# Kernel tuning notes

Measured on AMD Instinct MI355X. Metric: run time of the kernel, lower is better.

The kernel has to match this reference:

```python
import jax, jax.numpy as jnp
import numpy as np

Q_DIM = 9   # state(7) + action(2)
KV_DIM = 5  # fixed by get_input_tensors: 4 relative features + r_trans
H = 3
D = KV_DIM * H  # 15


def setup_inputs() -> dict:
    key = jax.random.key(0)
    ks = jax.random.split(key, 16)
    b, t = 32, 256

    def u(k, shape, fan_in):
        lim = (1.0 / fan_in) ** 0.5
        return jax.random.uniform(k, shape, jnp.float32, -lim, lim)

    return {
        "state": jax.random.normal(ks[0], (b, t, 7), jnp.float32),
        "action": jax.random.normal(ks[1], (b, t, 2), jnp.float32),
        "Wk": u(ks[2], (D, KV_DIM), KV_DIM),
        "Wq": u(ks[3], (D, Q_DIM), Q_DIM),
        "Wv": u(ks[4], (D, KV_DIM), KV_DIM),
        "att_bias": jax.random.uniform(ks[5], (KV_DIM,), jnp.float32, -0.1, 0.1),
        "Wscore": u(ks[6], (1, KV_DIM), KV_DIM),
        "bscore": u(ks[7], (1,), KV_DIM),
        "g1": jnp.ones((D,), jnp.float32),
        "beta1": jnp.zeros((D,), jnp.float32),
        "W1": u(ks[8], (5 * D, D), D),
        "bff1": u(ks[9], (5 * D,), D),
        "W2": u(ks[10], (D, 5 * D), 5 * D),
        "bff2": u(ks[11], (D,), 5 * D),
        "g2": jnp.ones((D,), jnp.float32),
        "beta2": jnp.zeros((D,), jnp.float32),
    }


def _layernorm(x, g, b, eps=1e-5):
    m = jnp.mean(x, axis=-1, keepdims=True)
    v = jnp.var(x, axis=-1, keepdims=True)
    return (x - m) * jax.lax.rsqrt(v + eps) * g + b


def _get_input_tensors(state):
    b, t, _ = state.shape
    init = state[..., :4]                                  # (b,t,4)
    rel = init[:, None, :, :] - init[:, :, None, :]        # (b,t,t,4): row i, col j -> s_j - s_i
    xy = rel.reshape(b, t, t, 2, 2).transpose(0, 1, 2, 4, 3)  # [...,0,:]=(x,vx), [...,1,:]=(y,vy)
    ang = -state[..., -1] + 0.5 * jnp.pi                   # (b,t)
    c = jnp.cos(ang)[:, None, :, None]                     # broadcast over row dim -> angle of col j
    s = jnp.sin(ang)[:, None, :, None]
    xr = xy[..., 0, :] * c - xy[..., 1, :] * s             # (b,t,t,2)
    yr = xy[..., 0, :] * s + xy[..., 1, :] * c
    rel = jnp.concatenate([xr, yr], axis=3)                # [xn,vxn,yn,vyn]
    rel = rel.reshape(b, t, t, 2, 2).transpose(0, 1, 2, 4, 3).reshape(b, t, t, 4)  # [xn,yn,vxn,vyn]
    # drop diagonal (j != i) via precomputed off-diagonal column indices
    rows = jnp.arange(t)[:, None]
    j = jnp.arange(t - 1)[None, :]
    cols = j + (j >= rows)                                 # (t,t-1)
    rel = rel[:, rows, cols, :]                            # (b,t,t-1,4)
    r = jnp.sqrt(rel[..., 0] ** 2 + rel[..., 1] ** 2)[..., None]  # (b,t,t-1,1)
    r_trans = 1.0 / (1.0 + jnp.exp(-1.0 + 5.0 * (r - 0.2)))
    kv_x = jnp.concatenate([rel[..., :2] / r, rel[..., 2:], r_trans], axis=-1)  # (b,t,t-1,5)
    return state, kv_x


def reference(state, action, Wk, Wq, Wv, att_bias, Wscore, bscore,
              g1, beta1, W1, bff1, W2, bff2, g2, beta2):
    q_x, kv_x = _get_input_tensors(state)
    q_x = jnp.concatenate([q_x, action], axis=-1)          # (b,t,Q_DIM)
    b, t, tm1, _ = kv_x.shape

    keys = (kv_x @ Wk.T).reshape(b, t, tm1, H, KV_DIM)     # (b,t,t-1,h,k)
    queries = (q_x @ Wq.T).reshape(b, t, 1, H, KV_DIM)
    e = jnp.tanh(keys + queries + att_bias)
    score = (e @ Wscore.T + bscore)[..., 0]                # (b,t,t-1,h)
    values = (kv_x @ Wv.T).reshape(b, t, tm1, H, KV_DIM)
    w = jax.nn.softmax(score, axis=2)                      # softmax over the t-1 neighbours
    x = jnp.einsum('btjh,btjhk->bthk', w, values).reshape(b, t, H * KV_DIM)

    x = _layernorm(x, g1, beta1)
    y = jax.nn.relu(x @ W1.T + bff1) @ W2.T + bff2
    x = x + y
    return _layernorm(x, g2, beta2)
```

## Files before the change

kernel.cpp:

```cpp
#include <hip/hip_runtime.h>
#include <math.h>

#define TT   256
#define TM1  255
#define QD   9
#define KD   5
#define NH   3
#define DD   15
#define HID  75
#define NR   18

__device__ __forceinline__ float fast_rcp(float x) {
    return __builtin_amdgcn_rcpf(x);
}

template<int CTRL>
__device__ __forceinline__ float dpp_add(float x) {
    int y = __builtin_amdgcn_update_dpp(0, __float_as_int(x), CTRL, 0xf, 0xf, true);
    return x + __int_as_float(y);
}

__device__ __forceinline__ float wave_sum63(float x) {
    x = dpp_add<0x111>(x);
    x = dpp_add<0x112>(x);
    x = dpp_add<0x114>(x);
    x = dpp_add<0x118>(x);
    x = dpp_add<0x142>(x);
    x = dpp_add<0x143>(x);
    return x;
}

__device__ __forceinline__ float bcast(float x, int l) {
    return __int_as_float(__builtin_amdgcn_readlane(__float_as_int(x), l));
}

__global__ __launch_bounds__(256)
void fused_block_kernel(const float* __restrict__ state,
                        const float* __restrict__ action,
                        const float* __restrict__ Wk,
                        const float* __restrict__ Wq,
                        const float* __restrict__ Wv,
                        const float* __restrict__ att_bias,
                        const float* __restrict__ Wscore,
                        const float* __restrict__ bscore,
                        const float* __restrict__ g1,
                        const float* __restrict__ beta1,
                        const float* __restrict__ W1,
                        const float* __restrict__ bff1,
                        const float* __restrict__ W2,
                        const float* __restrict__ bff2,
                        const float* __restrict__ g2,
                        const float* __restrict__ beta2,
                        float* __restrict__ out)
{
    const int tid  = threadIdx.x;
    const int lane = tid & 63;
    const int wv   = __builtin_amdgcn_readfirstlane(tid >> 6);
    const int qgrp = blockIdx.x * 4 + wv;
    const int b    = qgrp >> 8;
    const int qi   = qgrp & 255;

    __shared__ float s_h[4][76];

    const float* __restrict__ sb  = state + (size_t)b*TT*7;
    const float* __restrict__ sti = sb + qi*7;
    const float si0 = sti[0], si1 = sti[1], si2 = sti[2], si3 = sti[3];

    float qv = 0.0f;
    if (lane < DD) {
        float acc = att_bias[lane % KD];
        #pragma unroll
        for (int k = 0; k < 7; k++) acc = fmaf(Wq[lane*QD+k], sti[k], acc);
        acc = fmaf(Wq[lane*QD+7], action[((size_t)b*TT+qi)*2 + 0], acc);
        acc = fmaf(Wq[lane*QD+8], action[((size_t)b*TT+qi)*2 + 1], acc);
        qv = acc;
    }
    float qb2[DD];
    #pragma unroll
    for (int d = 0; d < DD; d++) qb2[d] = bcast(qv + qv, d);

    float wsc2[KD];
    float C = bscore[0];
    #pragma unroll
    for (int kk = 0; kk < KD; kk++) { float w = Wscore[kk]; wsc2[kk] = -2.0f*w; C += w; }

    float red[NR];
    #pragma unroll
    for (int n = 0; n < NR; n++) red[n] = 0.0f;

    #pragma unroll
    for (int pp = 0; pp < 4; pp++) {
        const int mm = lane + pp*64;
        if (mm < TM1) {
            const int jj = mm + (mm >= qi ? 1 : 0);
            const float* stj = sb + jj*7;
            const float d0 = stj[0]-si0, d1 = stj[1]-si1;
            const float d2 = stj[2]-si2, d3 = stj[3]-si3;
            const float th = stj[6];
            const float cs = __sinf(th);
            const float sn = __cosf(th);
            const float xr0 = d0*cs - d1*sn, yr0 = d0*sn + d1*cs;
            const float xr1 = d2*cs - d3*sn, yr1 = d2*sn + d3*cs;
            const float s2   = fmaxf(fmaf(xr0, xr0, yr0*yr0), 1e-12f);
            const float rinv = __builtin_amdgcn_rsqf(s2);
            const float r    = s2 * rinv;
            const float rt   = fast_rcp(1.0f + __expf(fmaf(5.0f, r, -2.0f)));
            const float kv0 = xr0*rinv, kv1 = yr0*rinv;
            const float f0 = kv0+kv0, f1 = kv1+kv1, f2 = xr1+xr1,
                        f3 = yr1+yr1, f4 = rt+rt;

            #pragma unroll
            for (int h = 0; h < NH; h++) {
                float sc = C;
                #pragma unroll
                for (int kk = 0; kk < KD; kk++) {
                    const int d = h*KD + kk;
                    float a = qb2[d];
                    a = fmaf(Wk[d*KD+0], f0, a);
                    a = fmaf(Wk[d*KD+1], f1, a);
                    a = fmaf(Wk[d*KD+2], f2, a);
                    a = fmaf(Wk[d*KD+3], f3, a);
                    a = fmaf(Wk[d*KD+4], f4, a);
                    sc = fmaf(wsc2[kk], fast_rcp(__expf(a) + 1.0f), sc);
                }
                const float p = __expf(sc);
                red[h] += p;
                red[NH+h*KD+0] = fmaf(p, kv0, red[NH+h*KD+0]);
                red[NH+h*KD+1] = fmaf(p, kv1, red[NH+h*KD+1]);
                red[NH+h*KD+2] = fmaf(p, xr1, red[NH+h*KD+2]);
                red[NH+h*KD+3] = fmaf(p, yr1, red[NH+h*KD+3]);
                red[NH+h*KD+4] = fmaf(p, rt , red[NH+h*KD+4]);
            }
        }
    }

    #pragma unroll
    for (int n = 0; n < NR; n++) red[n] = wave_sum63(red[n]);
    float fin[NR];
    #pragma unroll
    for (int n = 0; n < NR; n++) fin[n] = bcast(red[n], 63);

    float xm = 0.0f;
    if (lane < DD) {
        const int h = lane / KD;
        float acc = 0.0f;
        #pragma unroll
        for (int c = 0; c < KD; c++) acc = fmaf(Wv[lane*KD+c], fin[NH+h*KD+c], acc);
        xm = acc * fast_rcp(fin[h]);
    }

    float s1 = xm, sq = xm*xm;
    #pragma unroll
    for (int off = 8; off >= 1; off >>= 1) {
        s1 += __shfl_xor(s1, off, 16);
        sq += __shfl_xor(sq, off, 16);
    }
    const float mu1   = s1 * (1.0f/DD);
    const float rstd1 = rsqrtf(sq * (1.0f/DD) - mu1*mu1 + 1e-5f);
    float xln = 0.0f;
    if (lane < DD) xln = (xm - mu1) * rstd1 * g1[lane] + beta1[lane];

    float xs[DD];
    #pragma unroll
    for (int d = 0; d < DD; d++) xs[d] = bcast(xln, d);

    {
        float h0 = bff1[lane];
        #pragma unroll
        for (int k = 0; k < DD; k++) h0 = fmaf(W1[lane*DD+k], xs[k], h0);
        s_h[wv][lane] = fmaxf(h0, 0.0f);
        if (lane < HID-64) {
            float h1 = bff1[lane+64];
            #pragma unroll
            for (int k = 0; k < DD; k++) h1 = fmaf(W1[(lane+64)*DD+k], xs[k], h1);
            s_h[wv][lane+64] = fmaxf(h1, 0.0f);
        }
    }

    const int c2  = lane >> 4;
    const int d2c = lane & 15;
    const int cc  = (c2 < 3) ? c2 : 2;
    const int dc  = (d2c < DD) ? d2c : 0;
    float acc2 = 0.0f;
    #pragma unroll
    for (int k = 0; k < 25; k++)
        acc2 = fmaf(W2[dc*HID + cc*25 + k], s_h[wv][cc*25 + k], acc2);
    acc2 = (c2 < 3) ? acc2 : 0.0f;
    acc2 += __shfl_xor(acc2, 16);
    acc2 += __shfl_xor(acc2, 32);

    float x2 = 0.0f;
    if (lane < DD) x2 = xln + bff2[lane] + acc2;
    float t1 = x2, t2 = x2*x2;
    #pragma unroll
    for (int off = 8; off >= 1; off >>= 1) {
        t1 += __shfl_xor(t1, off, 16);
        t2 += __shfl_xor(t2, off, 16);
    }
    const float mu2   = t1 * (1.0f/DD);
    const float rstd2 = rsqrtf(t2 * (1.0f/DD) - mu2*mu2 + 1e-5f);
    if (lane < DD)
        out[(size_t)qgrp*DD + lane] = (x2 - mu2) * rstd2 * g2[lane] + beta2[lane];
}

extern "C" void kernel_launch(void* const* d_in, const int* in_sizes, int n_in,
                              void* d_out, int out_size, void* d_ws, size_t ws_size,
                              hipStream_t stream) {
    const float* state    = (const float*)d_in[0];
    const float* action   = (const float*)d_in[1];
    const float* Wk       = (const float*)d_in[2];
    const float* Wq       = (const float*)d_in[3];
    const float* Wv       = (const float*)d_in[4];
    const float* att_bias = (const float*)d_in[5];
    const float* Wscore   = (const float*)d_in[6];
    const float* bscore   = (const float*)d_in[7];
    const float* g1       = (const float*)d_in[8];
    const float* beta1    = (const float*)d_in[9];
    const float* W1       = (const float*)d_in[10];
    const float* bff1     = (const float*)d_in[11];
    const float* W2       = (const float*)d_in[12];
    const float* bff2     = (const float*)d_in[13];
    const float* g2       = (const float*)d_in[14];
    const float* beta2    = (const float*)d_in[15];
    float* out = (float*)d_out;

    dim3 grid(32 * 256 / 4);
    dim3 block(256);
    fused_block_kernel<<<grid, block, 0, stream>>>(
        state, action, Wk, Wq, Wv, att_bias, Wscore, bscore,
        g1, beta1, W1, bff1, W2, bff2, g2, beta2, out);
}
```

Before: 27.84 us.

## Fold exp scaling constants into features and hoist neighbor loads out of loop

Pre-scales queries, key features and score weights by 2*log2(e) so every exp becomes a raw v_exp_f32 (exp2) with no per-call multiply. Undoes the scale in the final value normalization. All neighbor state rows are loaded up front and features computed before the main loop. The masked tail lanes now use a large negative score constant instead of a branch. This trims VALU work per element and lets global loads overlap, at the cost of more live registers and a softmax tail contribution of exp2(-100) instead of exactly zero.

```diff
diff --git a/kernel.cpp b/kernel.cpp
--- a/kernel.cpp
+++ b/kernel.cpp
@@ -10,8 +10,16 @@
 #define HID  75
 #define NR   18
 
+#define K2E  2.8853900817779268f
+#define L2E  1.4426950408889634f
+#define INVK 0.34657359027997264f
+
 __device__ __forceinline__ float fast_rcp(float x) {
     return __builtin_amdgcn_rcpf(x);
+}
+
+__device__ __forceinline__ float exp2_raw(float x) {
+    float r; asm("v_exp_f32 %0, %1" : "=v"(r) : "v"(x)); return r;
 }
 
 template<int CTRL>
@@ -64,6 +72,18 @@
 
     const float* __restrict__ sb  = state + (size_t)b*TT*7;
     const float* __restrict__ sti = sb + qi*7;
+
+    float row[4][7];
+    #pragma unroll
+    for (int pp = 0; pp < 4; pp++) {
+        const int mmp = lane + pp*64;
+        int jj = mmp + (mmp >= qi ? 1 : 0);
+        jj = (jj < TT) ? jj : (TT-1);
+        const float* stj = sb + jj*7;
+        #pragma unroll
+        for (int k = 0; k < 7; k++) row[pp][k] = stj[k];
+    }
+
     const float si0 = sti[0], si1 = sti[1], si2 = sti[2], si3 = sti[3];
 
     float qv = 0.0f;
@@ -73,16 +93,42 @@
         for (int k = 0; k < 7; k++) acc = fmaf(Wq[lane*QD+k], sti[k], acc);
         acc = fmaf(Wq[lane*QD+7], action[((size_t)b*TT+qi)*2 + 0], acc);
         acc = fmaf(Wq[lane*QD+8], action[((size_t)b*TT+qi)*2 + 1], acc);
-        qv = acc;
+        qv = acc * K2E;
     }
     float qb2[DD];
     #pragma unroll
-    for (int d = 0; d < DD; d++) qb2[d] = bcast(qv + qv, d);
-
-    float wsc2[KD];
-    float C = bscore[0];
-    #pragma unroll
-    for (int kk = 0; kk < KD; kk++) { float w = Wscore[kk]; wsc2[kk] = -2.0f*w; C += w; }
+    for (int d = 0; d < DD; d++) qb2[d] = bcast(qv, d);
+
+    float w2[KD];
+    float Cn = bscore[0];
+    #pragma unroll
+    for (int kk = 0; kk < KD; kk++) { float w = Wscore[kk]; w2[kk] = -K2E*w; Cn += w; }
+    const float C2 = L2E * Cn;
+
+    float f0[4], f1[4], f2[4], f3[4], f4[4], Cp[4];
+    #pragma unroll
+    for (int pp = 0; pp < 4; pp++) {
+        const float d0 = row[pp][0]-si0, d1 = row[pp][1]-si1;
+        const float d2 = row[pp][2]-si2, d3 = row[pp][3]-si3;
+        const float th = row[pp][6];
+        const float cs = __sinf(th);
+        const float sn = __cosf(th);
+        const float xr0 = d0*cs - d1*sn, yr0 = d0*sn + d1*cs;
+        const float xr1 = d2*cs - d3*sn, yr1 = d2*sn + d3*cs;
+        const float s2   = fmaxf(fmaf(xr0, xr0, yr0*yr0), 1e-12f);
+        const float rinv = __builtin_amdgcn_rsqf(s2);
+        const float r    = s2 * rinv;
+        const float rt   = fast_rcp(1.0f + exp2_raw(fmaf(7.213475204444817f, r,
+                                                         -2.8853900817779268f)));
+        const float t = K2E * rinv;
+        f0[pp] = t * xr0;
+        f1[pp] = t * yr0;
+        f2[pp] = K2E * xr1;
+        f3[pp] = K2E * yr1;
+        f4[pp] = K2E * rt;
+        const int mm = lane + pp*64;
+        Cp[pp] = (mm < TM1) ? C2 : -100.0f;
+    }
 
     float red[NR];
     #pragma unroll
@@ -90,47 +136,27 @@
 
     #pragma unroll
     for (int pp = 0; pp < 4; pp++) {
-        const int mm = lane + pp*64;
-        if (mm < TM1) {
-            const int jj = mm + (mm >= qi ? 1 : 0);
-            const float* stj = sb + jj*7;
-            const float d0 = stj[0]-si0, d1 = stj[1]-si1;
-            const float d2 = stj[2]-si2, d3 = stj[3]-si3;
-            const float th = stj[6];
-            const float cs = __sinf(th);
-            const float sn = __cosf(th);
-            const float xr0 = d0*cs - d1*sn, yr0 = d0*sn + d1*cs;
-            const float xr1 = d2*cs - d3*sn, yr1 = d2*sn + d3*cs;
-            const float s2   = fmaxf(fmaf(xr0, xr0, yr0*yr0), 1e-12f);
-            const float rinv = __builtin_amdgcn_rsqf(s2);
-            const float r    = s2 * rinv;
-            const float rt   = fast_rcp(1.0f + __expf(fmaf(5.0f, r, -2.0f)));
-            const float kv0 = xr0*rinv, kv1 = yr0*rinv;
-            const float f0 = kv0+kv0, f1 = kv1+kv1, f2 = xr1+xr1,
-                        f3 = yr1+yr1, f4 = rt+rt;
-
+        #pragma unroll
+        for (int h = 0; h < NH; h++) {
+            float sc = Cp[pp];
             #pragma unroll
-            for (int h = 0; h < NH; h++) {
-                float sc = C;
-                #pragma unroll
-                for (int kk = 0; kk < KD; kk++) {
-                    const int d = h*KD + kk;
-                    float a = qb2[d];
-                    a = fmaf(Wk[d*KD+0], f0, a);
-                    a = fmaf(Wk[d*KD+1], f1, a);
-                    a = fmaf(Wk[d*KD+2], f2, a);
-                    a = fmaf(Wk[d*KD+3], f3, a);
-                    a = fmaf(Wk[d*KD+4], f4, a);
-                    sc = fmaf(wsc2[kk], fast_rcp(__expf(a) + 1.0f), sc);
-                }
-                const float p = __expf(sc);
-                red[h] += p;
-                red[NH+h*KD+0] = fmaf(p, kv0, red[NH+h*KD+0]);
-                red[NH+h*KD+1] = fmaf(p, kv1, red[NH+h*KD+1]);
-                red[NH+h*KD+2] = fmaf(p, xr1, red[NH+h*KD+2]);
-                red[NH+h*KD+3] = fmaf(p, yr1, red[NH+h*KD+3]);
-                red[NH+h*KD+4] = fmaf(p, rt , red[NH+h*KD+4]);
+            for (int kk = 0; kk < KD; kk++) {
+                const int d = h*KD + kk;
+                float a = qb2[d];
+                a = fmaf(Wk[d*KD+0], f0[pp], a);
+                a = fmaf(Wk[d*KD+1], f1[pp], a);
+                a = fmaf(Wk[d*KD+2], f2[pp], a);
+                a = fmaf(Wk[d*KD+3], f3[pp], a);
+                a = fmaf(Wk[d*KD+4], f4[pp], a);
+                sc = fmaf(w2[kk], fast_rcp(exp2_raw(a) + 1.0f), sc);
             }
+            const float p = exp2_raw(sc);
+            red[h] += p;
+            red[NH+h*KD+0] = fmaf(p, f0[pp], red[NH+h*KD+0]);
+            red[NH+h*KD+1] = fmaf(p, f1[pp], red[NH+h*KD+1]);
+            red[NH+h*KD+2] = fmaf(p, f2[pp], red[NH+h*KD+2]);
+            red[NH+h*KD+3] = fmaf(p, f3[pp], red[NH+h*KD+3]);
+            red[NH+h*KD+4] = fmaf(p, f4[pp], red[NH+h*KD+4]);
         }
     }
 
@@ -146,7 +172,7 @@
         float acc = 0.0f;
         #pragma unroll
         for (int c = 0; c < KD; c++) acc = fmaf(Wv[lane*KD+c], fin[NH+h*KD+c], acc);
-        xm = acc * fast_rcp(fin[h]);
+        xm = acc * fast_rcp(fin[h]) * INVK;
     }
 
     float s1 = xm, sq = xm*xm;
```

After: 26.30 us. -5.5%, faster.
